# Kernel optimization log

Hardware: AMD Instinct MI355X
Metric: run time of the kernel (lower is better)

The kernel has to match this reference:

```python
import jax, jax.numpy as jnp
import numpy as np

B, NL, NH, NG, NC, GOI = 1024, 64, 32, 20000, 64, 1000
EPS = 1e-5


def setup_inputs() -> dict:
    key = jax.random.key(0)
    ks = jax.random.split(key, 8)
    latent = jax.random.normal(ks[0], (B, NL), dtype=jnp.float32)
    genes_oi = jax.random.randint(ks[1], (GOI,), 0, NG, dtype=jnp.int64)
    W = jax.random.normal(ks[2], (NL, NH), dtype=jnp.float32) / np.sqrt(NL)
    b = jnp.zeros((NH,), dtype=jnp.float32)
    bn_gamma = jnp.ones((NH,), dtype=jnp.float32)
    bn_beta = jnp.zeros((NH,), dtype=jnp.float32)
    bn_mean = jnp.zeros((NH,), dtype=jnp.float32)
    bn_var = jnp.ones((NH,), dtype=jnp.float32)
    logit_table = jax.random.normal(ks[3], (NG, NH, NC), dtype=jnp.float32) * 0.02
    rho_table = jax.random.uniform(ks[4], (NG, NH), dtype=jnp.float32,
                                   minval=-1.0 / np.sqrt(NH), maxval=1.0 / np.sqrt(NH))
    return {"latent": latent, "genes_oi": genes_oi, "W": W, "b": b,
            "bn_gamma": bn_gamma, "bn_beta": bn_beta, "bn_mean": bn_mean,
            "bn_var": bn_var, "logit_table": logit_table, "rho_table": rho_table}


def reference(latent, genes_oi, W, b, bn_gamma, bn_beta, bn_mean, bn_var,
              logit_table, rho_table):
    # MLP: Linear -> BatchNorm1d (eval, running stats) -> ReLU (dropout off in eval)
    h = latent @ W + b                                      # [B, NH]
    h = (h - bn_mean) * jax.lax.rsqrt(bn_var + EPS) * bn_gamma + bn_beta
    h = jax.nn.relu(h)
    # sparse gather of per-gene weight tensors, then batched small matmul
    lw = logit_table[genes_oi]                              # [GOI, NH, NC]
    logit = jnp.einsum('bh,ghc->bgc', h, lw)                # [B, GOI, NC]
    rho = h @ rho_table.T                                   # [B, NG] (full weight)
    return (logit, rho)
```

## Files before the change

### kernel.cpp

```cpp
#include <hip/hip_runtime.h>

#define BATCH 1024
#define NL    64
#define NH    32
#define NG    20000
#define NC    64
#define GOI   1000

#define GPB          4
#define LOGIT_BLOCKS ((GOI / GPB) * 4)
#define RHO_NGRP     ((NG + 63) / 64)
#define RHO_YB       (BATCH / 64)
#define RHO_BLOCKS   (RHO_NGRP * RHO_YB)

typedef __attribute__((ext_vector_type(8))) short  short8;
typedef __attribute__((ext_vector_type(4))) float  f32x4;

static __device__ __forceinline__ unsigned short f2bf(float f) {
    unsigned int u = __builtin_bit_cast(unsigned int, f);
    unsigned int r = (u + 0x7fffu + ((u >> 16) & 1u)) >> 16;
    return (unsigned short)r;
}

__global__ __launch_bounds__(256) void h_kernel(
    const float* __restrict__ latent,
    const float* __restrict__ W,
    const float* __restrict__ bias,
    const float* __restrict__ gamma,
    const float* __restrict__ beta,
    const float* __restrict__ mean,
    const float* __restrict__ var,
    unsigned short* __restrict__ h)
{
    int tid = blockIdx.x * 256 + threadIdx.x;
    int b = tid >> 5;
    int k = tid & 31;
    float acc = 0.f;
    #pragma unroll 8
    for (int j = 0; j < NL; ++j)
        acc += latent[b * NL + j] * W[j * NH + k];
    acc += bias[k];
    float x = (acc - mean[k]) * rsqrtf(var[k] + 1e-5f) * gamma[k] + beta[k];
    x = fmaxf(x, 0.f);
    h[tid] = f2bf(x);
}

__global__ __launch_bounds__(256) void main_kernel(
    const unsigned short* __restrict__ h,
    const float*          __restrict__ ltab,
    const int*            __restrict__ genes,
    const float*          __restrict__ rtab,
    float*                __restrict__ out_logit,
    float*                __restrict__ out_rho)
{
    const int wave = threadIdx.x >> 6;
    const int lane = threadIdx.x & 63;
    const int l15  = lane & 15;
    const int quad = lane >> 4;
    const int bx   = blockIdx.x;

    if (bx < LOGIT_BLOCKS) {
        const int gt  = bx >> 2;
        const int ybl = bx & 3;
        const int g0  = gt * GPB;

        short8 bf[GPB][4];
        #pragma unroll
        for (int g = 0; g < GPB; ++g) {
            const long long gene = (long long)genes[g0 + g];
            const float* lw = ltab + gene * (long long)(NH * NC);
            #pragma unroll
            for (int t = 0; t < 4; ++t) {
                #pragma unroll
                for (int j = 0; j < 8; ++j)
                    bf[g][t][j] = (short)f2bf(lw[(quad * 8 + j) * NC + t * 16 + l15]);
            }
        }

        #pragma unroll
        for (int it = 0; it < 4; ++it) {
            const int b0 = ybl * 256 + it * 64 + wave * 16;
            short8 af = *(const short8*)(h + (b0 + l15) * NH + quad * 8);

            f32x4 acc[GPB][4];
            #pragma unroll
            for (int g = 0; g < GPB; ++g) {
                #pragma unroll
                for (int t = 0; t < 4; ++t) {
                    f32x4 z = {0.f, 0.f, 0.f, 0.f};
                    acc[g][t] = __builtin_amdgcn_mfma_f32_16x16x32_bf16(af, bf[g][t], z, 0, 0, 0);
                }
            }

            #pragma unroll
            for (int r = 0; r < 4; ++r) {
                const long long b = b0 + quad * 4 + r;
                float* op = out_logit + (b * GOI + g0) * NC + l15;
                #pragma unroll
                for (int g = 0; g < GPB; ++g) {
                    #pragma unroll
                    for (int t = 0; t < 4; ++t)
                        op[g * NC + t * 16] = acc[g][t][r];
                }
            }
        }
    } else {
        const int rb = bx - LOGIT_BLOCKS;
        const int yb = rb & 15;
        const int ng = rb >> 4;
        const int b0 = yb * 64 + wave * 16;

        short8 af = *(const short8*)(h + (b0 + l15) * NH + quad * 8);

        f32x4 acc[4];
        #pragma unroll
        for (int t = 0; t < 4; ++t) {
            const int n0 = ng * 64 + t * 16;
            if (n0 < NG) {
                const float* rp = rtab + (long long)(n0 + l15) * NH + quad * 8;
                short8 bfr;
                #pragma unroll
                for (int j = 0; j < 8; ++j)
                    bfr[j] = (short)f2bf(rp[j]);
                f32x4 z = {0.f, 0.f, 0.f, 0.f};
                acc[t] = __builtin_amdgcn_mfma_f32_16x16x32_bf16(af, bfr, z, 0, 0, 0);
            }
        }

        #pragma unroll
        for (int r = 0; r < 4; ++r) {
            const long long b = b0 + quad * 4 + r;
            float* op = out_rho + b * NG + ng * 64 + l15;
            #pragma unroll
            for (int t = 0; t < 4; ++t) {
                if (ng * 64 + t * 16 < NG)
                    op[t * 16] = acc[t][r];
            }
        }
    }
}

extern "C" void kernel_launch(void* const* d_in, const int* in_sizes, int n_in,
                              void* d_out, int out_size, void* d_ws, size_t ws_size,
                              hipStream_t stream) {
    const float* latent = (const float*)d_in[0];
    const int*   genes  = (const int*)d_in[1];
    const float* W      = (const float*)d_in[2];
    const float* bias   = (const float*)d_in[3];
    const float* gamma  = (const float*)d_in[4];
    const float* beta   = (const float*)d_in[5];
    const float* mean   = (const float*)d_in[6];
    const float* var    = (const float*)d_in[7];
    const float* ltab   = (const float*)d_in[8];
    const float* rtab   = (const float*)d_in[9];

    float* out = (float*)d_out;
    unsigned short* h = (unsigned short*)d_ws;

    float* out_logit = out;
    float* out_rho   = out + (long long)BATCH * GOI * NC;

    h_kernel<<<dim3((BATCH * NH) / 256), 256, 0, stream>>>(
        latent, W, bias, gamma, beta, mean, var, h);

    main_kernel<<<dim3(LOGIT_BLOCKS + RHO_BLOCKS), 256, 0, stream>>>(
        h, ltab, genes, rtab, out_logit, out_rho);
}
```

Before: 502.1 us.

## Swap MFMA operands to emit vectorized 16-byte output stores, one gene per block

After: 476.7 us. 1.05x faster.

```diff
diff --git a/kernel.cpp b/kernel.cpp
--- a/kernel.cpp
+++ b/kernel.cpp
@@ -7,8 +7,7 @@
 #define NC    64
 #define GOI   1000
 
-#define GPB          4
-#define LOGIT_BLOCKS ((GOI / GPB) * 4)
+#define LOGIT_BLOCKS (GOI * 4)
 #define RHO_NGRP     ((NG + 63) / 64)
 #define RHO_YB       (BATCH / 64)
 #define RHO_BLOCKS   (RHO_NGRP * RHO_YB)
@@ -60,21 +59,18 @@
     const int bx   = blockIdx.x;
 
     if (bx < LOGIT_BLOCKS) {
-        const int gt  = bx >> 2;
+        const int g   = bx >> 2;
         const int ybl = bx & 3;
-        const int g0  = gt * GPB;
 
-        short8 bf[GPB][4];
+        const long long gene = (long long)genes[g];
+        const float* lw = ltab + gene * (long long)(NH * NC);
+
+        short8 bf[4];
         #pragma unroll
-        for (int g = 0; g < GPB; ++g) {
-            const long long gene = (long long)genes[g0 + g];
-            const float* lw = ltab + gene * (long long)(NH * NC);
+        for (int t = 0; t < 4; ++t) {
             #pragma unroll
-            for (int t = 0; t < 4; ++t) {
-                #pragma unroll
-                for (int j = 0; j < 8; ++j)
-                    bf[g][t][j] = (short)f2bf(lw[(quad * 8 + j) * NC + t * 16 + l15]);
-            }
+            for (int j = 0; j < 8; ++j)
+                bf[t][j] = (short)f2bf(lw[(quad * 8 + j) * NC + t * 16 + l15]);
         }
 
         #pragma unroll
@@ -82,27 +78,18 @@
             const int b0 = ybl * 256 + it * 64 + wave * 16;
             short8 af = *(const short8*)(h + (b0 + l15) * NH + quad * 8);
 
-            f32x4 acc[GPB][4];
+            f32x4 acc[4];
             #pragma unroll
-            for (int g = 0; g < GPB; ++g) {
-                #pragma unroll
-                for (int t = 0; t < 4; ++t) {
-                    f32x4 z = {0.f, 0.f, 0.f, 0.f};
-                    acc[g][t] = __builtin_amdgcn_mfma_f32_16x16x32_bf16(af, bf[g][t], z, 0, 0, 0);
-                }
+            for (int t = 0; t < 4; ++t) {
+                f32x4 z = {0.f, 0.f, 0.f, 0.f};
+                acc[t] = __builtin_amdgcn_mfma_f32_16x16x32_bf16(bf[t], af, z, 0, 0, 0);
             }
 
+            float* op = out_logit +
+                ((long long)(b0 + l15) * GOI + g) * NC + quad * 4;
             #pragma unroll
-            for (int r = 0; r < 4; ++r) {
-                const long long b = b0 + quad * 4 + r;
-                float* op = out_logit + (b * GOI + g0) * NC + l15;
-                #pragma unroll
-                for (int g = 0; g < GPB; ++g) {
-                    #pragma unroll
-                    for (int t = 0; t < 4; ++t)
-                        op[g * NC + t * 16] = acc[g][t][r];
-                }
-            }
+            for (int t = 0; t < 4; ++t)
+                *(f32x4*)(op + t * 16) = acc[t];
         }
     } else {
         const int rb = bx - LOGIT_BLOCKS;
@@ -112,7 +99,6 @@
 
         short8 af = *(const short8*)(h + (b0 + l15) * NH + quad * 8);
 
-        f32x4 acc[4];
         #pragma unroll
         for (int t = 0; t < 4; ++t) {
             const int n0 = ng * 64 + t * 16;
@@ -123,18 +109,10 @@
                 for (int j = 0; j < 8; ++j)
                     bfr[j] = (short)f2bf(rp[j]);
                 f32x4 z = {0.f, 0.f, 0.f, 0.f};
-                acc[t] = __builtin_amdgcn_mfma_f32_16x16x32_bf16(af, bfr, z, 0, 0, 0);
-            }
-        }
-
-        #pragma unroll
-        for (int r = 0; r < 4; ++r) {
-            const long long b = b0 + quad * 4 + r;
-            float* op = out_rho + b * NG + ng * 64 + l15;
-            #pragma unroll
-            for (int t = 0; t < 4; ++t) {
-                if (ng * 64 + t * 16 < NG)
-                    op[t * 16] = acc[t][r];
+                f32x4 acc = __builtin_amdgcn_mfma_f32_16x16x32_bf16(bfr, af, z, 0, 0, 0);
+                float* op = out_rho +
+                    (long long)(b0 + l15) * NG + n0 + quad * 4;
+                *(f32x4*)op = acc;
             }
         }
     }
```
